# Kernel tuning notes

Hardware: AMD Instinct MI355X
Metric: run time of the kernel (lower is better)

Reference implementation:

```python
import jax, jax.numpy as jnp
import numpy as np

N_EMBD = 1024
N_HEAD = 16
HEAD_SIZE = N_EMBD // N_HEAD  # 64


def setup_inputs() -> dict:
    key = jax.random.key(0)
    k1, k2, k3, k4 = jax.random.split(key, 4)
    B, T = 4, 4096
    x = jax.random.normal(k1, (B, T, N_EMBD), dtype=jnp.float32)
    scale = 1.0 / np.sqrt(N_EMBD)
    # Linear(n_embd, head_size, bias=False): store as [C, H] so projection is x @ W
    Wk = jax.random.normal(k2, (N_EMBD, HEAD_SIZE), dtype=jnp.float32) * scale
    Wq = jax.random.normal(k3, (N_EMBD, HEAD_SIZE), dtype=jnp.float32) * scale
    Wv = jax.random.normal(k4, (N_EMBD, HEAD_SIZE), dtype=jnp.float32) * scale
    decay_factor = jnp.array([-0.5], dtype=jnp.float32)
    return {"x": x, "Wk": Wk, "Wq": Wq, "Wv": Wv, "decay_factor": decay_factor}


def reference(x, Wk, Wq, Wv, decay_factor):
    B, T, C = x.shape
    H = Wk.shape[1]
    k = x @ Wk  # [B,T,H]
    q = x @ Wq  # [B,T,H]
    v = x @ Wv  # [B,T,H]
    wei = jnp.einsum('bth,bsh->bts', q, k) * (H ** -0.5)  # [B,T,T]
    idx = jnp.arange(T)
    dist = jnp.minimum(idx[None, :] - idx[:, None], 0)  # j - i, clamped max=0
    ripple_bias = dist.astype(x.dtype) * jnp.abs(decay_factor[0])
    wei = wei + ripple_bias[None, :, :]
    causal = idx[None, :] <= idx[:, None]  # tril mask [T,T]
    wei = jnp.where(causal[None, :, :], wei, -jnp.inf)
    wei = jax.nn.softmax(wei, axis=-1)
    return jnp.einsum('bts,bsh->bth', wei, v)
```

## Files before the change

### kernel.cpp

```cpp
#include <hip/hip_runtime.h>

typedef short bf16x8 __attribute__((ext_vector_type(8)));
typedef float f32x4 __attribute__((ext_vector_type(4)));

#define TT 4096
#define CC 1024
#define HH 64
#define MTOT 16384

static __device__ __forceinline__ unsigned short f2bf(float f) {
  unsigned int u = __float_as_uint(f);
  unsigned int r = (u + 0x7FFFu + ((u >> 16) & 1u)) >> 16;
  return (unsigned short)r;
}

static __device__ __forceinline__ unsigned int pack_bf2(float lo, float hi) {
  unsigned int ul = __float_as_uint(lo) + 0x8000u;
  unsigned int uh = __float_as_uint(hi) + 0x8000u;
  return __builtin_amdgcn_perm(uh, ul, 0x07060302u);
}

typedef const __attribute__((address_space(1))) void gvoid;
typedef __attribute__((address_space(3))) void svoid;
static __device__ __forceinline__ void gll16(const void* g, void* l) {
  __builtin_amdgcn_global_load_lds((gvoid*)g, (svoid*)l, 16, 0, 0);
}

#define WAITVM(N) asm volatile("s_waitcnt vmcnt(" #N ")" ::: "memory")

__global__ void prep_wt(const float* __restrict__ Wk, const float* __restrict__ Wq,
                        const float* __restrict__ Wv, unsigned short* __restrict__ Wt) {
  __shared__ float T[64][65];
  const int mat = blockIdx.x >> 4;
  const int kt = blockIdx.x & 15;
  const float* src = (mat == 0) ? Wk : ((mat == 1) ? Wq : Wv);
#pragma unroll
  for (int i = 0; i < 4; ++i) {
    int c = i * 256 + threadIdx.x;
    int row = c >> 4, col = (c & 15) * 4;
    f32x4 v = *(const f32x4*)&src[(size_t)(kt * 64 + row) * HH + col];
    T[col + 0][row] = v[0];
    T[col + 1][row] = v[1];
    T[col + 2][row] = v[2];
    T[col + 3][row] = v[3];
  }
  __syncthreads();
#pragma unroll
  for (int i = 0; i < 2; ++i) {
    int c2 = i * 256 + threadIdx.x;
    int row = c2 >> 3, k0 = (c2 & 7) * 8;
    union { bf16x8 v; unsigned short h[8]; } pk;
#pragma unroll
    for (int j = 0; j < 8; ++j) pk.h[j] = f2bf(T[row][k0 + j]);
    *(bf16x8*)&Wt[(size_t)(mat * 64 + row) * CC + kt * 64 + k0] = pk.v;
  }
}

__global__ __launch_bounds__(512, 2) void proj_kernel(
    const float* __restrict__ x, const unsigned short* __restrict__ Wt,
    unsigned short* __restrict__ kb, unsigned short* __restrict__ qb,
    unsigned short* __restrict__ vt) {
  extern __shared__ __align__(16) char smem[];
  float* Xl = (float*)smem;
  unsigned short* Bl = (unsigned short*)(smem + 49152);

  const int tid = threadIdx.x;
  const int lane = tid & 63;
  const int w = tid >> 6;
  const int r = lane & 15, g = lane >> 4;
  const int rowgrp = w >> 1;
  const int colbase = (w & 1) * 96;
  const int m0 = blockIdx.x * 64;

  const float* xsrcs[2];
#pragma unroll
  for (int j = 0; j < 2; ++j) {
    int c = j * 512 + tid;
    int row = c >> 4, s = c & 15;
    xsrcs[j] = x + (size_t)(m0 + row) * CC + (((s & 8) | ((s & 7) ^ (row & 7))) * 4);
  }
  const unsigned short* bsrcs[3];
#pragma unroll
  for (int j = 0; j < 3; ++j) {
    int cb = j * 512 + tid;
    int row = cb >> 3, s = cb & 7;
    bsrcs[j] = Wt + (size_t)row * CC + ((s ^ (row & 7)) * 8);
  }

  f32x4 acc[6];
#pragma unroll
  for (int n = 0; n < 6; ++n) { f32x4 z = {0.f, 0.f, 0.f, 0.f}; acc[n] = z; }

  auto stage = [&](int t, int buf) {
    float* xb = Xl + buf * 4096;
    unsigned short* bb = Bl + buf * 12288;
#pragma unroll
    for (int j = 0; j < 2; ++j)
      gll16(xsrcs[j] + t * 64, xb + (j * 512 + w * 64) * 4);
#pragma unroll
    for (int j = 0; j < 3; ++j)
      gll16(bsrcs[j] + t * 64, bb + (size_t)(j * 512 + w * 64) * 8);
  };

  const int rr = rowgrp * 16 + r;
  const int rb = rr * 64;
  const int rx = rr & 7;

  auto body = [&](int buf) {
    const float* xb = Xl + buf * 4096;
    const unsigned short* bb = Bl + buf * 12288;
    bf16x8 bfr[2][6];
#pragma unroll
    for (int ks = 0; ks < 2; ++ks)
#pragma unroll
      for (int n = 0; n < 6; ++n) {
        int col = colbase + 16 * n + r;
        bfr[ks][n] = *(const bf16x8*)&bb[col * 64 + (((ks * 4 + g) ^ (col & 7)) * 8)];
      }
#pragma unroll
    for (int ks = 0; ks < 2; ++ks) {
      int s0 = ks * 8 + 2 * g;
      f32x4 v0 = *(const f32x4*)&xb[rb + (((s0 & 8) | ((s0 & 7) ^ rx)) * 4)];
      f32x4 v1 = *(const f32x4*)&xb[rb + ((((s0 + 1) & 8) | (((s0 + 1) & 7) ^ rx)) * 4)];
      union { bf16x8 v; unsigned int u[4]; } af;
      af.u[0] = pack_bf2(v0.x, v0.y);
      af.u[1] = pack_bf2(v0.z, v0.w);
      af.u[2] = pack_bf2(v1.x, v1.y);
      af.u[3] = pack_bf2(v1.z, v1.w);
#pragma unroll
      for (int n = 0; n < 6; ++n)
        acc[n] = __builtin_amdgcn_mfma_f32_16x16x32_bf16(af.v, bfr[ks][n], acc[n], 0, 0, 0);
    }
  };

  stage(0, 0);
  stage(1, 1);
  stage(2, 2);

  int buf = 0;
  for (int t = 0; t < 13; ++t) {
    WAITVM(10);
    __builtin_amdgcn_s_barrier();
    body(buf);
    __builtin_amdgcn_s_barrier();
    stage(t + 3, buf);
    buf = (buf == 2) ? 0 : buf + 1;
  }
  WAITVM(10); __builtin_amdgcn_s_barrier(); body(1);
  WAITVM(5);  __builtin_amdgcn_s_barrier(); body(2);
  WAITVM(0);  __builtin_amdgcn_s_barrier(); body(0);

#pragma unroll
  for (int n = 0; n < 6; ++n) {
#pragma unroll
    for (int i = 0; i < 4; ++i) {
      int row = m0 + rowgrp * 16 + 4 * g + i;
      int col = colbase + 16 * n + r;
      unsigned short h = f2bf(acc[n][i]);
      if (col < 64) {
        kb[(size_t)row * HH + col] = h;
      } else if (col < 128) {
        qb[(size_t)row * HH + (col - 64)] = h;
      } else {
        int dim = col - 128;
        int b = row >> 12;
        int tt = row & (TT - 1);
        vt[(((size_t)b * HH + dim) << 12) + tt] = h;
      }
    }
  }
}

__global__ __launch_bounds__(256, 2) void attn_kernel(
    const unsigned short* __restrict__ qb, const unsigned short* __restrict__ kb,
    const unsigned short* __restrict__ vt, const float* __restrict__ decayp,
    float* __restrict__ out) {
  extern __shared__ __align__(16) char smem[];
  unsigned short* Kl = (unsigned short*)smem;
  unsigned short* Vl = Kl + 16384;
  unsigned short* Pl = Vl + 16384;
  float* Ol = (float*)(smem + 65536);
  float* Ml = (float*)(smem + 65536 + 8704);
  float* Ll = Ml + 32;

  const int tid = threadIdx.x;
  const int lane = tid & 63;
  const int w = tid >> 6;
  const int r = lane & 15, g = lane >> 4;
  const int qh = w & 1;
  const int kvg = w >> 1;

  const int batch = blockIdx.x & 3;
  const int qt = blockIdx.x >> 2;
  const int qbase = qt * 32;
  const int qw = qbase + qh * 16;
  const int qrow = qw + r;

  const float decay = fabsf(decayp[0]);

  const unsigned short* qbb = qb + (size_t)batch * TT * HH;
  const unsigned short* kbb = kb + (size_t)batch * TT * HH;
  const unsigned short* vbb = vt + (size_t)batch * HH * TT;

  const unsigned short* qp = qbb + (size_t)qrow * HH;
  bf16x8 aq0 = *(const bf16x8*)(qp + 8 * g);
  bf16x8 aq1 = *(const bf16x8*)(qp + 32 + 8 * g);

  int t0 = 0;
  if (decay > 1e-8f) {
    float wf = 60.f / decay;
    if (wf < (float)TT) {
      int W = (int)wf + 1;
      int lo = qbase - W;
      if (lo < 0) lo = 0;
      t0 = lo >> 6;
    }
  }
  const int t1 = (qbase + 31) >> 6;
  const int nsteps = (t1 - t0 + 2) >> 1;

  const unsigned short* ksrc[4];
  const unsigned short* vsrc[4];
#pragma unroll
  for (int j = 0; j < 4; ++j) {
    int c = j * 256 + tid;
    int th = c >> 9;
    int cc = c & 511;
    int row = cc >> 3, sl = cc & 7;
    ksrc[j] = kbb + (size_t)((t0 + th) * 64 + row) * HH + ((sl ^ (row & 7)) * 8);
    vsrc[j] = vbb + (size_t)row * TT + (t0 + th) * 64 + ((sl ^ (row & 7)) * 8);
  }

  auto stage = [&](int s, int buf) {
#pragma unroll
    for (int j = 0; j < 4; ++j) {
      gll16(ksrc[j] + (size_t)s * 8192, Kl + buf * 8192 + (j * 256 + w * 64) * 8);
      gll16(vsrc[j] + s * 128, Vl + buf * 8192 + (j * 256 + w * 64) * 8);
    }
  };

  float m = -1e30f, lsum = 0.f;
  f32x4 o[4];
#pragma unroll
  for (int n = 0; n < 4; ++n) { f32x4 z = {0.f, 0.f, 0.f, 0.f}; o[n] = z; }

  stage(0, 0);

  for (int s = 0; s < nsteps; ++s) {
    if (s + 1 < nsteps) { stage(s + 1, (s + 1) & 1); WAITVM(8); }
    else { WAITVM(0); }
    __builtin_amdgcn_s_barrier();

    const int myt = t0 + 2 * s + kvg;
    if (myt <= t1) {
      const unsigned short* Kb = Kl + (s & 1) * 8192 + kvg * 4096;
      const unsigned short* Vb = Vl + (s & 1) * 8192 + kvg * 4096;
      const int kv0 = myt * 64;

      f32x4 sacc[4];
      __builtin_amdgcn_s_setprio(1);
#pragma unroll
      for (int t = 0; t < 4; ++t) {
        f32x4 z = {0.f, 0.f, 0.f, 0.f};
        int kvr = 16 * t + r;
        bf16x8 b0 = *(const bf16x8*)&Kb[kvr * 64 + ((g ^ (kvr & 7)) * 8)];
        bf16x8 b1 = *(const bf16x8*)&Kb[kvr * 64 + (((4 + g) ^ (kvr & 7)) * 8)];
        z = __builtin_amdgcn_mfma_f32_16x16x32_bf16(b0, aq0, z, 0, 0, 0);
        sacc[t] = __builtin_amdgcn_mfma_f32_16x16x32_bf16(b1, aq1, z, 0, 0, 0);
      }
      __builtin_amdgcn_s_setprio(0);

      float p[4][4];
      float rmax = -1e30f;
#pragma unroll
      for (int t = 0; t < 4; ++t)
#pragma unroll
        for (int i = 0; i < 4; ++i) {
          int kv = kv0 + 16 * t + 4 * g + i;
          float sv = sacc[t][i] * 0.125f + decay * (float)(kv - qrow);
          if (kv > qrow) sv = -1e30f;
          p[t][i] = sv;
          rmax = fmaxf(rmax, sv);
        }
      rmax = fmaxf(rmax, __shfl_xor(rmax, 16));
      rmax = fmaxf(rmax, __shfl_xor(rmax, 32));
      float mn = fmaxf(m, rmax);
      float al = __expf(m - mn);
      m = mn;
      float rs = 0.f;
#pragma unroll
      for (int t = 0; t < 4; ++t)
#pragma unroll
        for (int i = 0; i < 4; ++i) {
          float e = __expf(p[t][i] - mn);
          p[t][i] = e;
          rs += e;
        }
      rs += __shfl_xor(rs, 16);
      rs += __shfl_xor(rs, 32);
      lsum = lsum * al + rs;
#pragma unroll
      for (int n = 0; n < 4; ++n) {
        o[n][0] *= al; o[n][1] *= al; o[n][2] *= al; o[n][3] *= al;
      }

      char* P = (char*)(Pl + w * 1024) + r * 128;
#pragma unroll
      for (int t = 0; t < 4; ++t) {
        uint2 u;
        u.x = pack_bf2(p[t][0], p[t][1]);
        u.y = pack_bf2(p[t][2], p[t][3]);
        *(uint2*)(P + ((t ^ (r & 3)) * 32) + g * 8) = u;
      }
      bf16x8 pb0 = *(const bf16x8*)(P + (((g >> 1) ^ (r & 3)) * 32) + (g & 1) * 16);
      bf16x8 pb1 = *(const bf16x8*)(P + ((((g >> 1) + 2) ^ (r & 3)) * 32) + (g & 1) * 16);

      __builtin_amdgcn_s_setprio(1);
#pragma unroll
      for (int n = 0; n < 4; ++n) {
        int dim = 16 * n + r;
        bf16x8 v0 = *(const bf16x8*)&Vb[dim * 64 + ((g ^ (dim & 7)) * 8)];
        bf16x8 v1 = *(const bf16x8*)&Vb[dim * 64 + (((4 + g) ^ (dim & 7)) * 8)];
        o[n] = __builtin_amdgcn_mfma_f32_16x16x32_bf16(v0, pb0, o[n], 0, 0, 0);
        o[n] = __builtin_amdgcn_mfma_f32_16x16x32_bf16(v1, pb1, o[n], 0, 0, 0);
      }
      __builtin_amdgcn_s_setprio(0);
    }
    __builtin_amdgcn_s_barrier();
  }

  const int orow = qh * 16 + r;
  if (kvg == 1) {
    if (lane < 16) { Ml[orow] = m; Ll[orow] = lsum; }
#pragma unroll
    for (int n = 0; n < 4; ++n)
#pragma unroll
      for (int i = 0; i < 4; ++i)
        Ol[orow * 68 + 16 * n + 4 * g + i] = o[n][i];
  }
  __syncthreads();
  if (kvg == 0) {
    float m2 = Ml[orow], l2 = Ll[orow];
    float M = fmaxf(m, m2);
    float e1 = __expf(m - M), e2 = __expf(m2 - M);
    float inv = 1.f / (lsum * e1 + l2 * e2);
#pragma unroll
    for (int n = 0; n < 4; ++n)
#pragma unroll
      for (int i = 0; i < 4; ++i) {
        int d = 16 * n + 4 * g + i;
        Ol[orow * 68 + d] = (o[n][i] * e1 + Ol[orow * 68 + d] * e2) * inv;
      }
  }
  __syncthreads();

  float* ob = out + (size_t)batch * TT * HH;
#pragma unroll
  for (int j = 0; j < 2; ++j) {
    int c = j * 256 + tid;
    int row = c >> 4, q4 = (c & 15) * 4;
    f32x4 vv = *(const f32x4*)&Ol[row * 68 + q4];
    *(f32x4*)&ob[(size_t)(qbase + row) * HH + q4] = vv;
  }
}

extern "C" void kernel_launch(void* const* d_in, const int* in_sizes, int n_in,
                              void* d_out, int out_size, void* d_ws, size_t ws_size,
                              hipStream_t stream) {
  const float* x = (const float*)d_in[0];
  const float* Wk = (const float*)d_in[1];
  const float* Wq = (const float*)d_in[2];
  const float* Wv = (const float*)d_in[3];
  const float* decay = (const float*)d_in[4];
  float* out = (float*)d_out;

  unsigned short* kb = (unsigned short*)d_ws;
  unsigned short* qbw = kb + (size_t)MTOT * HH;
  unsigned short* vt = qbw + (size_t)MTOT * HH;
  unsigned short* Wt = vt + (size_t)MTOT * HH;

  prep_wt<<<dim3(48), dim3(256), 0, stream>>>(Wk, Wq, Wv, Wt);
  proj_kernel<<<dim3(256), dim3(512), 120 * 1024, stream>>>(x, Wt, kb, qbw, vt);
  attn_kernel<<<dim3(512), dim3(256), 74496, stream>>>(qbw, kb, vt, decay, out);
}
```

Measured before the change: 33.49 us.

## Use 32x32 MFMA tiles per wave and single-barrier pipeline in projection

The projection kernel now gives each of three waves a full 64x64 output tile, one each for K, Q and V, computed with 32x32x16 bf16 MFMAs. This raises operand reuse from LDS per MFMA compared with the previous 16x16 tiling spread across eight waves. The triple-buffered load loop now issues the next stage before compute and uses one barrier per iteration instead of two. The cost is that five of the eight waves only load data and do no math, which cuts compute parallelism inside each block. The output write is also remapped to the 32x32 accumulator layout.

```diff
diff --git a/kernel.cpp b/kernel.cpp
--- a/kernel.cpp
+++ b/kernel.cpp
@@ -2,6 +2,7 @@
 
 typedef short bf16x8 __attribute__((ext_vector_type(8)));
 typedef float f32x4 __attribute__((ext_vector_type(4)));
+typedef float f32x16 __attribute__((ext_vector_type(16)));
 
 #define TT 4096
 #define CC 1024
@@ -67,9 +68,8 @@
   const int tid = threadIdx.x;
   const int lane = tid & 63;
   const int w = tid >> 6;
-  const int r = lane & 15, g = lane >> 4;
-  const int rowgrp = w >> 1;
-  const int colbase = (w & 1) * 96;
+  const int l5 = lane >> 5;
+  const int l31 = lane & 31;
   const int m0 = blockIdx.x * 64;
 
   const float* xsrcs[2];
@@ -87,9 +87,13 @@
     bsrcs[j] = Wt + (size_t)row * CC + ((s ^ (row & 7)) * 8);
   }
 
-  f32x4 acc[6];
-#pragma unroll
-  for (int n = 0; n < 6; ++n) { f32x4 z = {0.f, 0.f, 0.f, 0.f}; acc[n] = z; }
+  f32x16 acc[2][2];
+#pragma unroll
+  for (int rt = 0; rt < 2; ++rt)
+#pragma unroll
+    for (int nt = 0; nt < 2; ++nt)
+#pragma unroll
+      for (int j = 0; j < 16; ++j) acc[rt][nt][j] = 0.f;
 
   auto stage = [&](int t, int buf) {
     float* xb = Xl + buf * 4096;
@@ -102,72 +106,73 @@
       gll16(bsrcs[j] + t * 64, bb + (size_t)(j * 512 + w * 64) * 8);
   };
 
-  const int rr = rowgrp * 16 + r;
-  const int rb = rr * 64;
-  const int rx = rr & 7;
+  const int rx = lane & 7;
+  const int colb = w * 64;
 
   auto body = [&](int buf) {
+    if (w >= 3) return;
     const float* xb = Xl + buf * 4096;
     const unsigned short* bb = Bl + buf * 12288;
-    bf16x8 bfr[2][6];
-#pragma unroll
-    for (int ks = 0; ks < 2; ++ks)
-#pragma unroll
-      for (int n = 0; n < 6; ++n) {
-        int col = colbase + 16 * n + r;
-        bfr[ks][n] = *(const bf16x8*)&bb[col * 64 + (((ks * 4 + g) ^ (col & 7)) * 8)];
-      }
-#pragma unroll
-    for (int ks = 0; ks < 2; ++ks) {
-      int s0 = ks * 8 + 2 * g;
-      f32x4 v0 = *(const f32x4*)&xb[rb + (((s0 & 8) | ((s0 & 7) ^ rx)) * 4)];
-      f32x4 v1 = *(const f32x4*)&xb[rb + ((((s0 + 1) & 8) | (((s0 + 1) & 7) ^ rx)) * 4)];
-      union { bf16x8 v; unsigned int u[4]; } af;
-      af.u[0] = pack_bf2(v0.x, v0.y);
-      af.u[1] = pack_bf2(v0.z, v0.w);
-      af.u[2] = pack_bf2(v1.x, v1.y);
-      af.u[3] = pack_bf2(v1.z, v1.w);
-#pragma unroll
-      for (int n = 0; n < 6; ++n)
-        acc[n] = __builtin_amdgcn_mfma_f32_16x16x32_bf16(af.v, bfr[ks][n], acc[n], 0, 0, 0);
+#pragma unroll
+    for (int ks = 0; ks < 4; ++ks) {
+      bf16x8 a[2];
+#pragma unroll
+      for (int rt = 0; rt < 2; ++rt) {
+        int row = rt * 32 + l31;
+        int s0 = ks * 4 + l5 * 2;
+        f32x4 v0 = *(const f32x4*)&xb[row * 64 + (((s0 & 8) | ((s0 & 7) ^ rx)) * 4)];
+        f32x4 v1 = *(const f32x4*)&xb[row * 64 + ((((s0 + 1) & 8) | (((s0 + 1) & 7) ^ rx)) * 4)];
+        union { bf16x8 v; unsigned int u[4]; } af;
+        af.u[0] = pack_bf2(v0.x, v0.y);
+        af.u[1] = pack_bf2(v0.z, v0.w);
+        af.u[2] = pack_bf2(v1.x, v1.y);
+        af.u[3] = pack_bf2(v1.z, v1.w);
+        a[rt] = af.v;
+      }
+#pragma unroll
+      for (int nt = 0; nt < 2; ++nt) {
+        int col = colb + nt * 32 + l31;
+        int slot = ks * 2 + l5;
+        bf16x8 b = *(const bf16x8*)&bb[col * 64 + ((slot ^ (col & 7)) * 8)];
+        acc[0][nt] = __builtin_amdgcn_mfma_f32_32x32x16_bf16(a[0], b, acc[0][nt], 0, 0, 0);
+        acc[1][nt] = __builtin_amdgcn_mfma_f32_32x32x16_bf16(a[1], b, acc[1][nt], 0, 0, 0);
+      }
     }
   };
 
   stage(0, 0);
   stage(1, 1);
-  stage(2, 2);
-
-  int buf = 0;
-  for (int t = 0; t < 13; ++t) {
-    WAITVM(10);
+
+  for (int t = 0; t < 15; ++t) {
+    WAITVM(5);
     __builtin_amdgcn_s_barrier();
-    body(buf);
-    __builtin_amdgcn_s_barrier();
-    stage(t + 3, buf);
-    buf = (buf == 2) ? 0 : buf + 1;
-  }
-  WAITVM(10); __builtin_amdgcn_s_barrier(); body(1);
-  WAITVM(5);  __builtin_amdgcn_s_barrier(); body(2);
-  WAITVM(0);  __builtin_amdgcn_s_barrier(); body(0);
-
-#pragma unroll
-  for (int n = 0; n < 6; ++n) {
-#pragma unroll
-    for (int i = 0; i < 4; ++i) {
-      int row = m0 + rowgrp * 16 + 4 * g + i;
-      int col = colbase + 16 * n + r;
-      unsigned short h = f2bf(acc[n][i]);
-      if (col < 64) {
-        kb[(size_t)row * HH + col] = h;
-      } else if (col < 128) {
-        qb[(size_t)row * HH + (col - 64)] = h;
-      } else {
-        int dim = col - 128;
-        int b = row >> 12;
-        int tt = row & (TT - 1);
-        vt[(((size_t)b * HH + dim) << 12) + tt] = h;
-      }
-    }
+    if (t + 2 < 16) stage(t + 2, (t + 2) % 3);
+    body(t % 3);
+  }
+  WAITVM(0);
+  __builtin_amdgcn_s_barrier();
+  body(0);
+
+  if (w < 3) {
+#pragma unroll
+    for (int rt = 0; rt < 2; ++rt)
+#pragma unroll
+      for (int nt = 0; nt < 2; ++nt)
+#pragma unroll
+        for (int j = 0; j < 16; ++j) {
+          int row = m0 + rt * 32 + (j & 3) + 8 * (j >> 2) + 4 * l5;
+          int cc = nt * 32 + l31;
+          unsigned short h = f2bf(acc[rt][nt][j]);
+          if (w == 0) {
+            kb[(size_t)row * HH + cc] = h;
+          } else if (w == 1) {
+            qb[(size_t)row * HH + cc] = h;
+          } else {
+            int b = row >> 12;
+            int tt = row & (TT - 1);
+            vt[(((size_t)b * HH + cc) << 12) + tt] = h;
+          }
+        }
   }
 }
 
```

New measurement: 42.62 us. +27.3%, slower.

## Restructure projection pipeline to single barrier per step and coalesce V-transpose stores

Applied to the files above, without the earlier changes.

The projection kernel's main loop now issues the next stage load before computing the current buffer, using one barrier per iteration instead of two and a prefetch distance of two over a three-buffer ring. The V output, previously written as scattered 2-byte transposed stores, is staged as fp32 in shared memory, converted to bf16 and written as 16-byte vectors along the time axis. This aims to cut barrier overhead and uncoalesced global writes, at the cost of extra LDS use and one more __syncthreads. Correctness depends on the staging reuse of smem at offset 73728 not overlapping live buffers, and on the single barrier being enough to keep stage(t+2) from overwriting the buffer read in body(t-1).

```diff
diff --git a/kernel.cpp b/kernel.cpp
--- a/kernel.cpp
+++ b/kernel.cpp
@@ -135,39 +135,43 @@
 
   stage(0, 0);
   stage(1, 1);
-  stage(2, 2);
-
-  int buf = 0;
-  for (int t = 0; t < 13; ++t) {
-    WAITVM(10);
+
+  for (int t = 0; t < 15; ++t) {
+    WAITVM(5);
     __builtin_amdgcn_s_barrier();
-    body(buf);
-    __builtin_amdgcn_s_barrier();
-    stage(t + 3, buf);
-    buf = (buf == 2) ? 0 : buf + 1;
-  }
-  WAITVM(10); __builtin_amdgcn_s_barrier(); body(1);
-  WAITVM(5);  __builtin_amdgcn_s_barrier(); body(2);
-  WAITVM(0);  __builtin_amdgcn_s_barrier(); body(0);
-
+    if (t + 2 < 16) stage(t + 2, (t + 2) % 3);
+    body(t % 3);
+  }
+  WAITVM(0);
+  __builtin_amdgcn_s_barrier();
+  body(0);
+
+  float* Vt = (float*)(smem + 73728);
 #pragma unroll
   for (int n = 0; n < 6; ++n) {
 #pragma unroll
     for (int i = 0; i < 4; ++i) {
-      int row = m0 + rowgrp * 16 + 4 * g + i;
+      int row = rowgrp * 16 + 4 * g + i;
       int col = colbase + 16 * n + r;
-      unsigned short h = f2bf(acc[n][i]);
+      float val = acc[n][i];
       if (col < 64) {
-        kb[(size_t)row * HH + col] = h;
+        kb[(size_t)(m0 + row) * HH + col] = f2bf(val);
       } else if (col < 128) {
-        qb[(size_t)row * HH + (col - 64)] = h;
+        qb[(size_t)(m0 + row) * HH + (col - 64)] = f2bf(val);
       } else {
-        int dim = col - 128;
-        int b = row >> 12;
-        int tt = row & (TT - 1);
-        vt[(((size_t)b * HH + dim) << 12) + tt] = h;
-      }
-    }
+        Vt[(col - 128) * 65 + row] = val;
+      }
+    }
+  }
+  __syncthreads();
+  {
+    int dim = tid >> 3, t8 = (tid & 7) * 8;
+    union { bf16x8 v; unsigned short h[8]; } pk;
+#pragma unroll
+    for (int j = 0; j < 8; ++j) pk.h[j] = f2bf(Vt[dim * 65 + t8 + j]);
+    int b = m0 >> 12;
+    int tt = (m0 & (TT - 1)) + t8;
+    *(bf16x8*)&vt[(((size_t)b * HH + dim) << 12) + tt] = pk.v;
   }
 }
 
```

Result: faster. 32.31 us (-3.5%).
